# Performance work log

Hardware: AMD Instinct MI355X
Metric: run time of the kernel (lower is better)

## Reference

```python
import jax, jax.numpy as jnp
import numpy as np

H = 0.01          # implicit time step from __init__
KS = 1000.0       # spring stiffness
CG_ITERS = 30     # fixed CG iteration count
EPS = 1e-8


def setup_inputs() -> dict:
    key = jax.random.key(0)
    k1, k2, k3, k4 = jax.random.split(key, 4)
    NV, NE = 200000, 1200000
    rhs = jax.random.normal(k1, (NV, 3), dtype=jnp.float32)
    pos = jax.random.uniform(k2, (NV, 3), dtype=jnp.float32)
    mass = jnp.ones((NV,), dtype=jnp.float32)
    rest_len = jax.random.uniform(k3, (NE,), dtype=jnp.float32) * 0.5 + 0.1
    edges = jax.random.randint(k4, (NE, 2), 0, NV, dtype=jnp.int32)
    return {"rhs": rhs, "pos": pos, "mass": mass, "rest_len": rest_len, "edges": edges}


def _spring_jacobians(pos, edges, rest_len):
    # Per-spring force Jacobian df_i/dx_i for f_i = -ks (|d| - l0) d_hat, d = x_i - x_j
    d = pos[edges[:, 0]] - pos[edges[:, 1]]            # (NE, 3)
    l = jnp.sqrt(jnp.sum(d * d, axis=-1)) + EPS        # (NE,)
    dhat = d / l[:, None]
    ddT = dhat[:, :, None] * dhat[:, None, :]          # (NE, 3, 3)
    I3 = jnp.eye(3, dtype=pos.dtype)
    coef = (1.0 - rest_len / l)[:, None, None]
    Jx = -KS * (coef * (I3 - ddT) + ddT)               # negative semidefinite
    return Jx


def _matvec(v, Jx, e0, e1, mass):
    # A v = M v - h^2 (dF/dx) v, assembled over the spring graph
    dv_e = v[e0] - v[e1]                               # (NE, 3)
    f_e = jnp.einsum('eij,ej->ei', Jx, dv_e)           # (NE, 3)
    Jv = jnp.zeros_like(v).at[e0].add(f_e).at[e1].add(-f_e)
    return mass[:, None] * v - (H * H) * Jv


def reference(rhs, pos, mass, rest_len, edges):
    # Implicit mass-spring step: solve (M - h^2 J) dv = rhs with fixed-iteration CG
    Jx = _spring_jacobians(pos, edges, rest_len)
    e0, e1 = edges[:, 0], edges[:, 1]

    def matvec(v):
        return _matvec(v, Jx, e0, e1, mass)

    b = rhs
    x0 = jnp.zeros_like(b)                             # dv.fill(0.0)
    rs0 = jnp.vdot(b, b)

    def cg_step(carry, _):
        x, r, p, rs = carry
        Ap = matvec(p)
        alpha = rs / (jnp.vdot(p, Ap) + EPS)
        x = x + alpha * p
        r = r - alpha * Ap
        rs_new = jnp.vdot(r, r)
        p = r + (rs_new / (rs + EPS)) * p
        return (x, r, p, rs_new), None

    (x, _, _, _), _ = jax.lax.scan(cg_step, (x0, b, b, rs0), None, length=CG_ITERS)
    return x
```

## Files before the change

### kernel.cpp

```cpp
#include <hip/hip_runtime.h>

#define CG_ITERS 30
#define PAP_OFF 32
#define TILE 8192
#define CHAIN_TB 256

__device__ __forceinline__ float fadd32(float a, float b){ return __fadd_rn(a,b); }
__device__ __forceinline__ float fsub32(float a, float b){ return __fsub_rn(a,b); }
__device__ __forceinline__ float fmul32(float a, float b){ return __fmul_rn(a,b); }
__device__ __forceinline__ float fdiv32(float a, float b){ return __fdiv_rn(a,b); }

__device__ __forceinline__ void edge_force(int2 e, int eidx,
                                           const float* __restrict__ pos,
                                           const float* __restrict__ rl,
                                           const float* __restrict__ p,
                                           float f[3]) {
    int i0 = 3 * e.x, i1 = 3 * e.y;
    float d[3], dh[3], dv[3];
    d[0] = fsub32(pos[i0 + 0], pos[i1 + 0]);
    d[1] = fsub32(pos[i0 + 1], pos[i1 + 1]);
    d[2] = fsub32(pos[i0 + 2], pos[i1 + 2]);
    float ss = fadd32(fadd32(fmul32(d[0], d[0]), fmul32(d[1], d[1])), fmul32(d[2], d[2]));
    float l  = fadd32(__fsqrt_rn(ss), 1e-8f);
    dh[0] = fdiv32(d[0], l); dh[1] = fdiv32(d[1], l); dh[2] = fdiv32(d[2], l);
    float coef = fsub32(1.0f, fdiv32(rl[eidx], l));
    dv[0] = fsub32(p[i0 + 0], p[i1 + 0]);
    dv[1] = fsub32(p[i0 + 1], p[i1 + 1]);
    dv[2] = fsub32(p[i0 + 2], p[i1 + 2]);
    #pragma unroll
    for (int i = 0; i < 3; ++i) {
        float acc = 0.0f;
        #pragma unroll
        for (int j = 2; j >= 0; --j) {
            float dd = fmul32(dh[i], dh[j]);
            float t  = (i == j) ? fsub32(1.0f, dd) : fsub32(0.0f, dd);
            float w  = fadd32(fmul32(coef, t), dd);
            float Jx = fmul32(-1000.0f, w);
            acc = fadd32(acc, fmul32(Jx, dv[j]));
        }
        f[i] = acc;
    }
}

__global__ void count_k(const int2* __restrict__ ed, int* __restrict__ cnt0,
                        int* __restrict__ cnt1, int ne) {
    int i = blockIdx.x * blockDim.x + threadIdx.x;
    if (i >= ne) return;
    int2 e = ed[i];
    atomicAdd(&cnt0[e.x], 1);
    atomicAdd(&cnt1[e.y], 1);
}

__global__ void scan_k(const int* __restrict__ cnt0, const int* __restrict__ cnt1,
                       int* __restrict__ segoff, int* __restrict__ split,
                       int* __restrict__ cur0, int* __restrict__ cur1, int nv) {
    __shared__ int lds[1024];
    int tid = threadIdx.x;
    int chunk = (nv + 1023) / 1024;
    int lo = tid * chunk;
    int hi = lo + chunk; if (hi > nv) hi = nv; if (lo > nv) lo = nv;
    int s = 0;
    for (int v = lo; v < hi; ++v) s += cnt0[v] + cnt1[v];
    lds[tid] = s;
    __syncthreads();
    for (int off = 1; off < 1024; off <<= 1) {
        int t = (tid >= off) ? lds[tid - off] : 0;
        __syncthreads();
        lds[tid] += t;
        __syncthreads();
    }
    int run = lds[tid] - s;
    for (int v = lo; v < hi; ++v) {
        int c0 = cnt0[v], c1 = cnt1[v];
        segoff[v] = run;
        split[v]  = run + c0;
        cur0[v]   = run;
        cur1[v]   = run + c0;
        run += c0 + c1;
    }
    if (tid == 1023) segoff[nv] = lds[1023];
}

__global__ void fill_k(const int2* __restrict__ ed, int* __restrict__ cur0,
                       int* __restrict__ cur1, int* __restrict__ inc, int ne) {
    int i = blockIdx.x * blockDim.x + threadIdx.x;
    if (i >= ne) return;
    int2 e = ed[i];
    int s0 = atomicAdd(&cur0[e.x], 1); inc[s0] = i;
    int s1 = atomicAdd(&cur1[e.y], 1); inc[s1] = i;
}

__global__ void sort_k(int* __restrict__ inc, const int* __restrict__ segoff,
                       const int* __restrict__ split, int nv) {
    int v = blockIdx.x * blockDim.x + threadIdx.x;
    if (v >= nv) return;
    int lo = segoff[v], mid = split[v], hi = segoff[v + 1];
    for (int a = lo + 1; a < mid; ++a) {
        int key = inc[a]; int b = a - 1;
        while (b >= lo && inc[b] > key) { inc[b + 1] = inc[b]; --b; }
        inc[b + 1] = key;
    }
    for (int a = mid + 1; a < hi; ++a) {
        int key = inc[a]; int b = a - 1;
        while (b >= mid && inc[b] > key) { inc[b + 1] = inc[b]; --b; }
        inc[b + 1] = key;
    }
}

__global__ void init_k(const float* __restrict__ rhs, float* __restrict__ x,
                       float* __restrict__ r, float* __restrict__ p,
                       float* __restrict__ prod, int n) {
    int j = blockIdx.x * blockDim.x + threadIdx.x;
    if (j >= n) return;
    float b = rhs[j];
    x[j] = 0.0f; r[j] = b; p[j] = b;
    prod[j] = fmul32(b, b);
}

__global__ void mv_k(const int2* __restrict__ ed, const float* __restrict__ pos,
                     const float* __restrict__ rl, const float* __restrict__ p,
                     const float* __restrict__ mass, const int* __restrict__ inc,
                     const int* __restrict__ segoff, const int* __restrict__ split,
                     float* __restrict__ Ap, float* __restrict__ prod, int nv) {
    int v = blockIdx.x * blockDim.x + threadIdx.x;
    if (v >= nv) return;
    int lo = segoff[v], mid = split[v], hi = segoff[v + 1];
    float a0 = 0.0f, a1 = 0.0f, a2 = 0.0f;
    for (int k = lo; k < mid; ++k) {
        int e = inc[k]; float f[3];
        edge_force(ed[e], e, pos, rl, p, f);
        a0 = fadd32(a0, f[0]); a1 = fadd32(a1, f[1]); a2 = fadd32(a2, f[2]);
    }
    for (int k = mid; k < hi; ++k) {
        int e = inc[k]; float f[3];
        edge_force(ed[e], e, pos, rl, p, f);
        a0 = fadd32(a0, -f[0]); a1 = fadd32(a1, -f[1]); a2 = fadd32(a2, -f[2]);
    }
    const float h2 = (float)(0.01 * 0.01);
    int j = 3 * v; float m = mass[v];
    float p0 = p[j], p1 = p[j + 1], p2 = p[j + 2];
    float A0 = fsub32(fmul32(m, p0), fmul32(h2, a0));
    float A1 = fsub32(fmul32(m, p1), fmul32(h2, a1));
    float A2 = fsub32(fmul32(m, p2), fmul32(h2, a2));
    Ap[j + 0] = A0; Ap[j + 1] = A1; Ap[j + 2] = A2;
    prod[j + 0] = fmul32(p0, A0);
    prod[j + 1] = fmul32(p1, A1);
    prod[j + 2] = fmul32(p2, A2);
}

#define SCHED_FENCE() __builtin_amdgcn_sched_barrier(0)
#define ACC4(v) { s = fadd32(s, (v).x); s = fadd32(s, (v).y); \
                  s = fadd32(s, (v).z); s = fadd32(s, (v).w); }
#define G8_DECL(P) float4 P##0, P##1, P##2, P##3, P##4, P##5, P##6, P##7;
#define G8_LOAD(P, b4, base) { P##0=(b4)[(base)+0]; P##1=(b4)[(base)+1]; \
    P##2=(b4)[(base)+2]; P##3=(b4)[(base)+3]; P##4=(b4)[(base)+4]; \
    P##5=(b4)[(base)+5]; P##6=(b4)[(base)+6]; P##7=(b4)[(base)+7]; }
#define G8_ACC(P) { ACC4(P##0) ACC4(P##1) ACC4(P##2) ACC4(P##3) \
                    ACC4(P##4) ACC4(P##5) ACC4(P##6) ACC4(P##7) }

__global__ void __launch_bounds__(CHAIN_TB, 1)
chain_k(const float* __restrict__ prod, float* __restrict__ out, int n) {
    __shared__ float buf[2][TILE];
    int tid = threadIdx.x;
    int ntiles = (n + TILE - 1) / TILE;
    {
        int lim = (TILE < n) ? TILE : n;
        for (int i = tid; i < lim; i += CHAIN_TB) buf[0][i] = prod[i];
    }
    __syncthreads();
    float s = 0.0f;
    for (int t = 0; t < ntiles; ++t) {
        if (t + 1 < ntiles) {
            int base = (t + 1) * TILE;
            int lim = n - base; if (lim > TILE) lim = TILE;
            float* dst = buf[(t + 1) & 1];
            for (int i = tid; i < lim; i += CHAIN_TB) dst[i] = prod[base + i];
        }
        if (tid == 0) {
            const float* b = buf[t & 1];
            int cnt = n - t * TILE; if (cnt > TILE) cnt = TILE;
            const float4* b4 = (const float4*)b;
            int c4 = cnt >> 2;
            int ng = c4 >> 3;
            int g = 0;
            if (ng >= 5) {
                G8_DECL(A) G8_DECL(B) G8_DECL(C)
                G8_LOAD(A, b4, 0)
                SCHED_FENCE();
                G8_LOAD(B, b4, 8)
                SCHED_FENCE();
                for (; g + 5 <= ng; g += 3) {
                    G8_LOAD(C, b4, (g + 2) << 3)  SCHED_FENCE();
                    G8_ACC(A)                     SCHED_FENCE();
                    G8_LOAD(A, b4, (g + 3) << 3)  SCHED_FENCE();
                    G8_ACC(B)                     SCHED_FENCE();
                    G8_LOAD(B, b4, (g + 4) << 3)  SCHED_FENCE();
                    G8_ACC(C)                     SCHED_FENCE();
                }
                G8_ACC(A)
                G8_ACC(B)
                g += 2;
            }
            for (; g < ng; ++g) {
                G8_DECL(D)
                G8_LOAD(D, b4, g << 3)
                G8_ACC(D)
            }
            for (int i = ng << 3; i < c4; ++i) { float4 v = b4[i]; ACC4(v) }
            for (int k = c4 << 2; k < cnt; ++k) s = fadd32(s, b[k]);
        }
        __syncthreads();
    }
    if (tid == 0) out[0] = s;
}

__global__ void xr_k(float* __restrict__ x, float* __restrict__ r,
                     const float* __restrict__ p, const float* __restrict__ Ap,
                     float* __restrict__ prod, const float* __restrict__ scal,
                     int it, int n) {
    int j = blockIdx.x * blockDim.x + threadIdx.x;
    if (j >= n) return;
    float alpha = (float)((double)scal[it] / ((double)scal[PAP_OFF + it] + 1e-8));
    x[j] = fadd32(x[j], fmul32(alpha, p[j]));
    float rn = fsub32(r[j], fmul32(alpha, Ap[j]));
    r[j] = rn;
    prod[j] = fmul32(rn, rn);
}

__global__ void p_k(const float* __restrict__ r, float* __restrict__ p,
                    const float* __restrict__ scal, int it, int n) {
    int j = blockIdx.x * blockDim.x + threadIdx.x;
    if (j >= n) return;
    float beta = (float)((double)scal[it + 1] / ((double)scal[it] + 1e-8));
    p[j] = fadd32(r[j], fmul32(beta, p[j]));
}

extern "C" void kernel_launch(void* const* d_in, const int* in_sizes, int n_in,
                              void* d_out, int out_size, void* d_ws, size_t ws_size,
                              hipStream_t stream) {
    const float* rhs  = (const float*)d_in[0];
    const float* pos  = (const float*)d_in[1];
    const float* mass = (const float*)d_in[2];
    const float* rl   = (const float*)d_in[3];
    const int2*  ed   = (const int2*)d_in[4];
    float* x = (float*)d_out;

    int NV = in_sizes[0] / 3;
    int NE = in_sizes[3];
    int n3 = NV * 3;

    char* w = (char*)d_ws;
    float* r    = (float*)w;  w += (size_t)n3 * sizeof(float);
    float* p    = (float*)w;  w += (size_t)n3 * sizeof(float);
    float* Ap   = (float*)w;  w += (size_t)n3 * sizeof(float);
    float* prod = (float*)w;  w += (size_t)n3 * sizeof(float);
    int*   inc  = (int*)w;    w += (size_t)2 * NE * sizeof(int);
    int*   cnt0 = (int*)w;    w += (size_t)NV * sizeof(int);
    int*   cnt1 = (int*)w;    w += (size_t)NV * sizeof(int);
    int*   segoff = (int*)w;  w += (size_t)(NV + 1) * sizeof(int);
    int*   split  = (int*)w;  w += (size_t)NV * sizeof(int);
    int*   cur0   = (int*)w;  w += (size_t)NV * sizeof(int);
    int*   cur1   = (int*)w;  w += (size_t)NV * sizeof(int);
    float* scal   = (float*)w;

    hipMemsetAsync(cnt0, 0, (size_t)2 * NV * sizeof(int), stream);

    const int tb = 256;
    int gE = (NE + tb - 1) / tb;
    int gV = (NV + tb - 1) / tb;
    int g3 = (n3 + tb - 1) / tb;

    count_k<<<gE, tb, 0, stream>>>(ed, cnt0, cnt1, NE);
    scan_k<<<1, 1024, 0, stream>>>(cnt0, cnt1, segoff, split, cur0, cur1, NV);
    fill_k<<<gE, tb, 0, stream>>>(ed, cur0, cur1, inc, NE);
    sort_k<<<gV, tb, 0, stream>>>(inc, segoff, split, NV);

    init_k<<<g3, tb, 0, stream>>>(rhs, x, r, p, prod, n3);
    chain_k<<<1, CHAIN_TB, 0, stream>>>(prod, &scal[0], n3);

    for (int it = 0; it < CG_ITERS; ++it) {
        mv_k<<<gV, tb, 0, stream>>>(ed, pos, rl, p, mass, inc, segoff, split, Ap, prod, NV);
        chain_k<<<1, CHAIN_TB, 0, stream>>>(prod, &scal[PAP_OFF + it], n3);
        xr_k<<<g3, tb, 0, stream>>>(x, r, p, Ap, prod, scal, it, n3);
        if (it + 1 < CG_ITERS) {
            chain_k<<<1, CHAIN_TB, 0, stream>>>(prod, &scal[it + 1], n3);
            p_k<<<g3, tb, 0, stream>>>(r, p, scal, it, n3);
        }
    }
}
```

Before: 106.6 ms.

## Fuse serial dot-product reduction into producer kernels via per-tile ready counters

```diff
diff --git a/kernel.cpp b/kernel.cpp
--- a/kernel.cpp
+++ b/kernel.cpp
@@ -4,6 +4,7 @@
 #define PAP_OFF 32
 #define TILE 8192
 #define CHAIN_TB 256
+#define ROWSTRIDE 128
 
 __device__ __forceinline__ float fadd32(float a, float b){ return __fadd_rn(a,b); }
 __device__ __forceinline__ float fsub32(float a, float b){ return __fsub_rn(a,b); }
@@ -107,47 +108,6 @@
     }
 }
 
-__global__ void init_k(const float* __restrict__ rhs, float* __restrict__ x,
-                       float* __restrict__ r, float* __restrict__ p,
-                       float* __restrict__ prod, int n) {
-    int j = blockIdx.x * blockDim.x + threadIdx.x;
-    if (j >= n) return;
-    float b = rhs[j];
-    x[j] = 0.0f; r[j] = b; p[j] = b;
-    prod[j] = fmul32(b, b);
-}
-
-__global__ void mv_k(const int2* __restrict__ ed, const float* __restrict__ pos,
-                     const float* __restrict__ rl, const float* __restrict__ p,
-                     const float* __restrict__ mass, const int* __restrict__ inc,
-                     const int* __restrict__ segoff, const int* __restrict__ split,
-                     float* __restrict__ Ap, float* __restrict__ prod, int nv) {
-    int v = blockIdx.x * blockDim.x + threadIdx.x;
-    if (v >= nv) return;
-    int lo = segoff[v], mid = split[v], hi = segoff[v + 1];
-    float a0 = 0.0f, a1 = 0.0f, a2 = 0.0f;
-    for (int k = lo; k < mid; ++k) {
-        int e = inc[k]; float f[3];
-        edge_force(ed[e], e, pos, rl, p, f);
-        a0 = fadd32(a0, f[0]); a1 = fadd32(a1, f[1]); a2 = fadd32(a2, f[2]);
-    }
-    for (int k = mid; k < hi; ++k) {
-        int e = inc[k]; float f[3];
-        edge_force(ed[e], e, pos, rl, p, f);
-        a0 = fadd32(a0, -f[0]); a1 = fadd32(a1, -f[1]); a2 = fadd32(a2, -f[2]);
-    }
-    const float h2 = (float)(0.01 * 0.01);
-    int j = 3 * v; float m = mass[v];
-    float p0 = p[j], p1 = p[j + 1], p2 = p[j + 2];
-    float A0 = fsub32(fmul32(m, p0), fmul32(h2, a0));
-    float A1 = fsub32(fmul32(m, p1), fmul32(h2, a1));
-    float A2 = fsub32(fmul32(m, p2), fmul32(h2, a2));
-    Ap[j + 0] = A0; Ap[j + 1] = A1; Ap[j + 2] = A2;
-    prod[j + 0] = fmul32(p0, A0);
-    prod[j + 1] = fmul32(p1, A1);
-    prod[j + 2] = fmul32(p2, A2);
-}
-
 #define SCHED_FENCE() __builtin_amdgcn_sched_barrier(0)
 #define ACC4(v) { s = fadd32(s, (v).x); s = fadd32(s, (v).y); \
                   s = fadd32(s, (v).z); s = fadd32(s, (v).w); }
@@ -158,29 +118,56 @@
 #define G8_ACC(P) { ACC4(P##0) ACC4(P##1) ACC4(P##2) ACC4(P##3) \
                     ACC4(P##4) ACC4(P##5) ACC4(P##6) ACC4(P##7) }
 
-__global__ void __launch_bounds__(CHAIN_TB, 1)
-chain_k(const float* __restrict__ prod, float* __restrict__ out, int n) {
+__device__ __forceinline__ void mark_range(int* __restrict__ tilecnt,
+                                           int flo, int fhi) {
+    if (fhi <= flo) return;
+    __threadfence();
+    int t0 = flo / TILE, t1 = (fhi - 1) / TILE;
+    for (int t = t0; t <= t1; ++t) {
+        int lo = t * TILE;       if (lo < flo) lo = flo;
+        int hi = (t + 1) * TILE; if (hi > fhi) hi = fhi;
+        atomicAdd(&tilecnt[t], hi - lo);
+    }
+}
+
+__device__ void chain_consume(const float* __restrict__ prod,
+                              int* __restrict__ tilecnt,
+                              float* __restrict__ out, int n) {
     __shared__ float buf[2][TILE];
+    __shared__ int sgen;
     int tid = threadIdx.x;
     int ntiles = (n + TILE - 1) / TILE;
-    {
-        int lim = (TILE < n) ? TILE : n;
-        for (int i = tid; i < lim; i += CHAIN_TB) buf[0][i] = prod[i];
-    }
+    if (tid == 0) sgen = -1;
+    __syncthreads();
+
+#define WAITSTAGE(T) { \
+        int lim = n - (T) * TILE; if (lim > TILE) lim = TILE; \
+        if (tid == 1) { \
+            while (__hip_atomic_load(&tilecnt[(T)], __ATOMIC_ACQUIRE, \
+                                     __HIP_MEMORY_SCOPE_AGENT) < lim) \
+                __builtin_amdgcn_s_sleep(2); \
+            __hip_atomic_store(&sgen, (T), __ATOMIC_RELEASE, \
+                               __HIP_MEMORY_SCOPE_WORKGROUP); \
+        } \
+        while (__hip_atomic_load(&sgen, __ATOMIC_ACQUIRE, \
+                                 __HIP_MEMORY_SCOPE_WORKGROUP) < (T)) {} \
+        float* dst = buf[(T) & 1]; \
+        const float* src = prod + (size_t)(T) * TILE; \
+        for (int i = tid - 1; i < lim; i += (CHAIN_TB - 1)) \
+            dst[i] = __hip_atomic_load((const float*)&src[i], __ATOMIC_RELAXED, \
+                                       __HIP_MEMORY_SCOPE_AGENT); \
+    }
+
+    if (tid > 0) WAITSTAGE(0);
     __syncthreads();
     float s = 0.0f;
     for (int t = 0; t < ntiles; ++t) {
-        if (t + 1 < ntiles) {
-            int base = (t + 1) * TILE;
-            int lim = n - base; if (lim > TILE) lim = TILE;
-            float* dst = buf[(t + 1) & 1];
-            for (int i = tid; i < lim; i += CHAIN_TB) dst[i] = prod[base + i];
-        }
+        if (t + 1 < ntiles && tid > 0) WAITSTAGE(t + 1);
         if (tid == 0) {
             const float* b = buf[t & 1];
-            int cnt = n - t * TILE; if (cnt > TILE) cnt = TILE;
+            int cfl = n - t * TILE; if (cfl > TILE) cfl = TILE;
             const float4* b4 = (const float4*)b;
-            int c4 = cnt >> 2;
+            int c4 = cfl >> 2;
             int ng = c4 >> 3;
             int g = 0;
             if (ng >= 5) {
@@ -206,29 +193,113 @@
                 G8_LOAD(D, b4, g << 3)
                 G8_ACC(D)
             }
-            for (int i = ng << 3; i < c4; ++i) { float4 v = b4[i]; ACC4(v) }
-            for (int k = c4 << 2; k < cnt; ++k) s = fadd32(s, b[k]);
+            for (int i2 = ng << 3; i2 < c4; ++i2) { float4 v = b4[i2]; ACC4(v) }
+            for (int k2 = c4 << 2; k2 < cfl; ++k2) s = fadd32(s, b[k2]);
         }
         __syncthreads();
     }
     if (tid == 0) out[0] = s;
-}
-
-__global__ void xr_k(float* __restrict__ x, float* __restrict__ r,
-                     const float* __restrict__ p, const float* __restrict__ Ap,
-                     float* __restrict__ prod, const float* __restrict__ scal,
-                     int it, int n) {
-    int j = blockIdx.x * blockDim.x + threadIdx.x;
-    if (j >= n) return;
-    float alpha = (float)((double)scal[it] / ((double)scal[PAP_OFF + it] + 1e-8));
-    x[j] = fadd32(x[j], fmul32(alpha, p[j]));
-    float rn = fsub32(r[j], fmul32(alpha, Ap[j]));
-    r[j] = rn;
-    prod[j] = fmul32(rn, rn);
-}
-
-__global__ void p_k(const float* __restrict__ r, float* __restrict__ p,
-                    const float* __restrict__ scal, int it, int n) {
+#undef WAITSTAGE
+}
+
+
+__global__ void __launch_bounds__(CHAIN_TB, 1)
+initchain_k(const float* __restrict__ rhs, float* __restrict__ x,
+            float* __restrict__ r, float* __restrict__ p,
+            float* __restrict__ prod, int* __restrict__ tilecnt,
+            float* __restrict__ out, int n) {
+    if (blockIdx.x < gridDim.x - 1) {
+        int j = blockIdx.x * CHAIN_TB + threadIdx.x;
+        if (j < n) {
+            float b = rhs[j];
+            x[j] = 0.0f; r[j] = b; p[j] = b;
+            prod[j] = fmul32(b, b);
+        }
+        __syncthreads();
+        if (threadIdx.x == 0) {
+            int flo = blockIdx.x * CHAIN_TB;
+            int fhi = flo + CHAIN_TB; if (fhi > n) fhi = n;
+            mark_range(tilecnt, flo, fhi);
+        }
+    } else {
+        chain_consume(prod, tilecnt, out, n);
+    }
+}
+
+__global__ void __launch_bounds__(CHAIN_TB, 1)
+mvchain_k(const int2* __restrict__ ed, const float* __restrict__ pos,
+          const float* __restrict__ rl, const float* __restrict__ p,
+          const float* __restrict__ mass, const int* __restrict__ inc,
+          const int* __restrict__ segoff, const int* __restrict__ split,
+          float* __restrict__ Ap, float* __restrict__ prod,
+          int* __restrict__ tilecnt, float* __restrict__ out,
+          int nv, int n3) {
+    if (blockIdx.x < gridDim.x - 1) {
+        int v = blockIdx.x * CHAIN_TB + threadIdx.x;
+        if (v < nv) {
+            int lo = segoff[v], mid = split[v], hi = segoff[v + 1];
+            float a0 = 0.0f, a1 = 0.0f, a2 = 0.0f;
+            for (int k = lo; k < mid; ++k) {
+                int e = inc[k]; float f[3];
+                edge_force(ed[e], e, pos, rl, p, f);
+                a0 = fadd32(a0, f[0]); a1 = fadd32(a1, f[1]); a2 = fadd32(a2, f[2]);
+            }
+            for (int k = mid; k < hi; ++k) {
+                int e = inc[k]; float f[3];
+                edge_force(ed[e], e, pos, rl, p, f);
+                a0 = fadd32(a0, -f[0]); a1 = fadd32(a1, -f[1]); a2 = fadd32(a2, -f[2]);
+            }
+            const float h2 = (float)(0.01 * 0.01);
+            int j = 3 * v; float m = mass[v];
+            float p0 = p[j], p1 = p[j + 1], p2 = p[j + 2];
+            float A0 = fsub32(fmul32(m, p0), fmul32(h2, a0));
+            float A1 = fsub32(fmul32(m, p1), fmul32(h2, a1));
+            float A2 = fsub32(fmul32(m, p2), fmul32(h2, a2));
+            Ap[j + 0] = A0; Ap[j + 1] = A1; Ap[j + 2] = A2;
+            prod[j + 0] = fmul32(p0, A0);
+            prod[j + 1] = fmul32(p1, A1);
+            prod[j + 2] = fmul32(p2, A2);
+        }
+        __syncthreads();
+        if (threadIdx.x == 0) {
+            int vlo = blockIdx.x * CHAIN_TB;
+            int vhi = vlo + CHAIN_TB; if (vhi > nv) vhi = nv;
+            mark_range(tilecnt, 3 * vlo, 3 * vhi);
+        }
+    } else {
+        chain_consume(prod, tilecnt, out, n3);
+    }
+}
+
+__global__ void __launch_bounds__(CHAIN_TB, 1)
+xrchain_k(float* __restrict__ x, float* __restrict__ r,
+          const float* __restrict__ p, const float* __restrict__ Ap,
+          float* __restrict__ prod, const float* __restrict__ scal,
+          int it, int* __restrict__ tilecnt, float* __restrict__ out,
+          int do_chain, int n) {
+    if (blockIdx.x < gridDim.x - 1) {
+        int j = blockIdx.x * CHAIN_TB + threadIdx.x;
+        if (j < n) {
+            float alpha = (float)((double)scal[it] / ((double)scal[PAP_OFF + it] + 1e-8));
+            x[j] = fadd32(x[j], fmul32(alpha, p[j]));
+            float rn = fsub32(r[j], fmul32(alpha, Ap[j]));
+            r[j] = rn;
+            prod[j] = fmul32(rn, rn);
+        }
+        __syncthreads();
+        if (threadIdx.x == 0) {
+            int flo = blockIdx.x * CHAIN_TB;
+            int fhi = flo + CHAIN_TB; if (fhi > n) fhi = n;
+            mark_range(tilecnt, flo, fhi);
+        }
+    } else {
+        if (do_chain) chain_consume(prod, tilecnt, out, n);
+    }
+}
+
+__global__ void __launch_bounds__(256)
+p_k(const float* __restrict__ r, float* __restrict__ p,
+    const float* __restrict__ scal, int it, int n) {
     int j = blockIdx.x * blockDim.x + threadIdx.x;
     if (j >= n) return;
     float beta = (float)((double)scal[it + 1] / ((double)scal[it] + 1e-8));
@@ -261,9 +332,11 @@
     int*   split  = (int*)w;  w += (size_t)NV * sizeof(int);
     int*   cur0   = (int*)w;  w += (size_t)NV * sizeof(int);
     int*   cur1   = (int*)w;  w += (size_t)NV * sizeof(int);
-    float* scal   = (float*)w;
+    float* scal    = (float*)w; w += (size_t)64 * sizeof(float);
+    int*   tilecnt = (int*)w;
 
     hipMemsetAsync(cnt0, 0, (size_t)2 * NV * sizeof(int), stream);
+    hipMemsetAsync(tilecnt, 0, (size_t)64 * ROWSTRIDE * sizeof(int), stream);
 
     const int tb = 256;
     int gE = (NE + tb - 1) / tb;
@@ -275,15 +348,19 @@
     fill_k<<<gE, tb, 0, stream>>>(ed, cur0, cur1, inc, NE);
     sort_k<<<gV, tb, 0, stream>>>(inc, segoff, split, NV);
 
-    init_k<<<g3, tb, 0, stream>>>(rhs, x, r, p, prod, n3);
-    chain_k<<<1, CHAIN_TB, 0, stream>>>(prod, &scal[0], n3);
+    initchain_k<<<g3 + 1, CHAIN_TB, 0, stream>>>(rhs, x, r, p, prod,
+                                                 tilecnt, &scal[0], n3);
 
     for (int it = 0; it < CG_ITERS; ++it) {
-        mv_k<<<gV, tb, 0, stream>>>(ed, pos, rl, p, mass, inc, segoff, split, Ap, prod, NV);
-        chain_k<<<1, CHAIN_TB, 0, stream>>>(prod, &scal[PAP_OFF + it], n3);
-        xr_k<<<g3, tb, 0, stream>>>(x, r, p, Ap, prod, scal, it, n3);
-        if (it + 1 < CG_ITERS) {
-            chain_k<<<1, CHAIN_TB, 0, stream>>>(prod, &scal[it + 1], n3);
+        mvchain_k<<<gV + 1, CHAIN_TB, 0, stream>>>(ed, pos, rl, p, mass, inc,
+                                                   segoff, split, Ap, prod,
+                                                   tilecnt + (size_t)(1 + it) * ROWSTRIDE,
+                                                   &scal[PAP_OFF + it], NV, n3);
+        int doch = (it + 1 < CG_ITERS) ? 1 : 0;
+        xrchain_k<<<g3 + 1, CHAIN_TB, 0, stream>>>(x, r, p, Ap, prod, scal, it,
+                                                   tilecnt + (size_t)(32 + it) * ROWSTRIDE,
+                                                   &scal[it + 1], doch, n3);
+        if (doch) {
             p_k<<<g3, tb, 0, stream>>>(r, p, scal, it, n3);
         }
     }
```

Measured after the change: 141.4 ms. +32.6%, slower.
